# Optimization experiments

Measured on AMD Instinct MI355X. Metric: run time of the kernel, lower is better.

The kernel has to match this reference:

```python
import jax, jax.numpy as jnp
import numpy as np

EPS = 1.0 / 137.0  # fine-structure-constant epsilon used throughout the Yat ops


def yat_dense(x, W, b, alpha):
    # x: [..., C], W: [C, F] -> [..., F]
    dot = jnp.einsum('btc,cf->btf', x, W)
    x_norm = jnp.sum(x * x, axis=-1, keepdims=True)        # [..., 1]
    w_norm = jnp.sum(W * W, axis=0)                         # [F]
    dist = x_norm + w_norm - 2.0 * dot
    y = dot * dot / (dist + EPS)
    y = y + b
    F = W.shape[1]
    scale = (np.sqrt(F) / np.log(1.0 + F)) ** 1.0           # base; alpha exponent applied below
    return y * ((np.float32(np.sqrt(F)) / np.float32(np.log1p(F))) ** alpha)


def setup_inputs() -> dict:
    key = jax.random.key(0)
    ks = jax.random.split(key, 8)
    B, T, C = 4, 1024, 768
    x = jax.random.normal(ks[0], (B, T, C), dtype=jnp.float32)
    mask = jnp.tril(jnp.ones((T, T), dtype=bool))[None, None, :, :]  # causal [1,1,T,T]
    sd = 1.0 / np.sqrt(C)
    W_attn = jax.random.normal(ks[1], (C, 3 * C), dtype=jnp.float32) * sd
    b_attn = jnp.zeros((3 * C,), dtype=jnp.float32)
    alpha_attn = jnp.ones((), dtype=jnp.float32)
    W_proj = jax.random.normal(ks[2], (C, C), dtype=jnp.float32) * sd
    b_proj = jnp.zeros((C,), dtype=jnp.float32)
    alpha_proj = jnp.ones((), dtype=jnp.float32)
    return {"x": x, "mask": mask, "W_attn": W_attn, "b_attn": b_attn,
            "alpha_attn": alpha_attn, "W_proj": W_proj, "b_proj": b_proj,
            "alpha_proj": alpha_proj}


def reference(x, mask, W_attn, b_attn, alpha_attn, W_proj, b_proj, alpha_proj):
    B, T, C = x.shape
    H = 12
    D = C // H  # head_dim
    qkv = yat_dense(x, W_attn, b_attn, alpha_attn)          # [B,T,3C]
    qkv = qkv.reshape(B, T, 3 * H, D)
    q, k, v = jnp.array_split(qkv, 3, axis=2)
    q = jnp.transpose(q, (0, 2, 1, 3))                       # [B,H,T,D]
    k = jnp.transpose(k, (0, 2, 1, 3))
    v = jnp.transpose(v, (0, 2, 1, 3))
    scale = 1.0 / np.float32(np.sqrt(D))
    dot = jnp.einsum('bhid,bhjd->bhij', q, k)                # [B,H,T,T]
    sq_dot = jnp.square(dot * scale)
    q_norm = jnp.sum(jnp.square(q), axis=-1)[..., None]      # [B,H,T,1]
    k_norm = jnp.sum(jnp.square(k), axis=-1)[..., None, :]   # [B,H,1,T]
    sq_dist = q_norm + k_norm - 2.0 * dot * scale
    attn = sq_dot / (sq_dist + EPS)
    attn = jnp.where(mask, attn, jnp.finfo(jnp.float32).min)
    attn = jax.nn.softmax(attn, axis=-1)
    out = jnp.einsum('bhij,bhjd->bhid', attn, v)             # [B,H,T,D]
    out = jnp.transpose(out, (0, 2, 1, 3)).reshape(B, T, C)
    out = yat_dense(out, W_proj, b_proj, alpha_proj)         # [B,T,C]
    return out
```

## Files before the change

kernel.cpp:

```cpp
#include <hip/hip_runtime.h>
#include <math.h>

#define EPS_YAT (1.0f/137.0f)

typedef unsigned short u16;
typedef unsigned int u32;
typedef __attribute__((ext_vector_type(8))) __bf16 bf16x8;
typedef __attribute__((ext_vector_type(4))) float f32x4;

__device__ __forceinline__ float4 ld4(const float* p) { return *(const float4*)p; }

__device__ __forceinline__ u16 bf16_rne(float f) {
    u32 u = __float_as_uint(f);
    u32 r = (u + 0x7fffu + ((u >> 16) & 1u)) >> 16;
    return (u16)r;
}
__device__ __forceinline__ float bf16_f(u16 h) {
    return __uint_as_float(((u32)h) << 16);
}

__device__ __forceinline__ void glds16(const u16* g, u16* s) {
    __builtin_amdgcn_global_load_lds(
        (const __attribute__((address_space(1))) void*)g,
        (__attribute__((address_space(3))) void*)s,
        16, 0, 0);
}

__global__ void colnorm_part(const float* __restrict__ W, float* __restrict__ part,
                             int K, int N) {
    __shared__ float sm[256];
    const int col = blockIdx.x * 64 + (threadIdx.x & 63);
    const int q = threadIdx.x >> 6;
    const int rows = K >> 6;
    const int k0 = blockIdx.y * (K >> 4) + q * rows;
    float s = 0.f;
    for (int k = k0; k < k0 + rows; ++k) {
        float w = W[(size_t)k * N + col];
        s += w * w;
    }
    sm[threadIdx.x] = s;
    __syncthreads();
    if (threadIdx.x < 64)
        part[(size_t)blockIdx.y * N + col] =
            sm[threadIdx.x] + sm[threadIdx.x + 64] + sm[threadIdx.x + 128] + sm[threadIdx.x + 192];
}

__global__ void colnorm_reduce(const float* __restrict__ part, float* __restrict__ wn,
                               int N) {
    int gid = blockIdx.x * 256 + threadIdx.x;
    if (gid >= N) return;
    float s = 0.f;
    #pragma unroll
    for (int i = 0; i < 16; ++i) s += part[(size_t)i * N + gid];
    wn[gid] = s;
}

__global__ void split_rownorm(const float* __restrict__ X, u16* __restrict__ Xh,
                              u16* __restrict__ Xl, float* __restrict__ rn) {
    int wave = threadIdx.x >> 6;
    int lane = threadIdx.x & 63;
    int row = blockIdx.x * 4 + wave;
    const float* xr = X + (size_t)row * 768;
    u16* xh = Xh + (size_t)row * 768;
    u16* xl = Xl + (size_t)row * 768;
    float s = 0.f;
    #pragma unroll
    for (int k = lane * 4; k < 768; k += 256) {
        float4 v = ld4(xr + k);
        s += v.x * v.x + v.y * v.y + v.z * v.z + v.w * v.w;
        u16 h0 = bf16_rne(v.x), h1 = bf16_rne(v.y), h2 = bf16_rne(v.z), h3 = bf16_rne(v.w);
        u16 l0 = bf16_rne(v.x - bf16_f(h0));
        u16 l1 = bf16_rne(v.y - bf16_f(h1));
        u16 l2 = bf16_rne(v.z - bf16_f(h2));
        u16 l3 = bf16_rne(v.w - bf16_f(h3));
        uint2 hp, lp;
        hp.x = (u32)h0 | ((u32)h1 << 16); hp.y = (u32)h2 | ((u32)h3 << 16);
        lp.x = (u32)l0 | ((u32)l1 << 16); lp.y = (u32)l2 | ((u32)l3 << 16);
        *(uint2*)(xh + k) = hp;
        *(uint2*)(xl + k) = lp;
    }
    for (int off = 32; off; off >>= 1) s += __shfl_down(s, off);
    if (lane == 0) rn[row] = s;
}

__global__ void rownorm_hl(const u16* __restrict__ Xh, const u16* __restrict__ Xl,
                           float* __restrict__ rn) {
    int wave = threadIdx.x >> 6;
    int lane = threadIdx.x & 63;
    int row = blockIdx.x * 4 + wave;
    const u16* xh = Xh + (size_t)row * 768;
    const u16* xl = Xl + (size_t)row * 768;
    float s = 0.f;
    for (int k = lane * 4; k < 768; k += 256) {
        uint2 hv = *(const uint2*)(xh + k);
        uint2 lv = *(const uint2*)(xl + k);
        float a0 = bf16_f((u16)hv.x)         + bf16_f((u16)lv.x);
        float a1 = bf16_f((u16)(hv.x >> 16)) + bf16_f((u16)(lv.x >> 16));
        float a2 = bf16_f((u16)hv.y)         + bf16_f((u16)lv.y);
        float a3 = bf16_f((u16)(hv.y >> 16)) + bf16_f((u16)(lv.y >> 16));
        s += a0 * a0 + a1 * a1 + a2 * a2 + a3 * a3;
    }
    for (int off = 32; off; off >>= 1) s += __shfl_down(s, off);
    if (lane == 0) rn[row] = s;
}

__global__ void qknorm_kernel(const u16* __restrict__ qh, const u16* __restrict__ ql,
                              float* __restrict__ qn, float* __restrict__ kn) {
    int gid = blockIdx.x * 256 + threadIdx.x;
    int lane = gid & 15;
    int idx = gid >> 4;
    int which = (idx >= 49152) ? 1 : 0;
    int r = idx - which * 49152;
    int t = r & 1023;
    int bh = r >> 10;
    int h = bh % 12, b = bh / 12;
    const size_t off = (size_t)(b * 1024 + t) * 2304 + which * 768 + h * 64 + lane * 4;
    uint2 hv = *(const uint2*)(qh + off);
    uint2 lv = *(const uint2*)(ql + off);
    float a0 = bf16_f((u16)hv.x)         + bf16_f((u16)lv.x);
    float a1 = bf16_f((u16)(hv.x >> 16)) + bf16_f((u16)(lv.x >> 16));
    float a2 = bf16_f((u16)hv.y)         + bf16_f((u16)lv.y);
    float a3 = bf16_f((u16)(hv.y >> 16)) + bf16_f((u16)(lv.y >> 16));
    float s = a0 * a0 + a1 * a1 + a2 * a2 + a3 * a3;
    s += __shfl_xor(s, 1, 16);
    s += __shfl_xor(s, 2, 16);
    s += __shfl_xor(s, 4, 16);
    s += __shfl_xor(s, 8, 16);
    if (lane == 0) (which ? kn : qn)[r] = s;
}

__global__ void split_wt_kernel(const float* __restrict__ W, u16* __restrict__ Th,
                                u16* __restrict__ Tl, int K, int N) {
    __shared__ float tile[64 * 68];
    const int tid = threadIdx.x;
    const int n0 = blockIdx.x << 6;
    const int k0 = blockIdx.y << 6;
    const int rr = tid >> 4;
    const int cc = (tid & 15) << 2;
    #pragma unroll
    for (int s = 0; s < 4; ++s) {
        int k_l = rr + s * 16;
        *(float4*)&tile[k_l * 68 + cc] = ld4(W + (size_t)(k0 + k_l) * N + n0 + cc);
    }
    __syncthreads();
    #pragma unroll
    for (int s = 0; s < 4; ++s) {
        int n_l = rr + s * 16;
        float a0 = tile[(cc + 0) * 68 + n_l];
        float a1 = tile[(cc + 1) * 68 + n_l];
        float a2 = tile[(cc + 2) * 68 + n_l];
        float a3 = tile[(cc + 3) * 68 + n_l];
        u16 h0 = bf16_rne(a0), h1 = bf16_rne(a1), h2 = bf16_rne(a2), h3 = bf16_rne(a3);
        u16 l0 = bf16_rne(a0 - bf16_f(h0));
        u16 l1 = bf16_rne(a1 - bf16_f(h1));
        u16 l2 = bf16_rne(a2 - bf16_f(h2));
        u16 l3 = bf16_rne(a3 - bf16_f(h3));
        uint2 hp, lp;
        hp.x = (u32)h0 | ((u32)h1 << 16); hp.y = (u32)h2 | ((u32)h3 << 16);
        lp.x = (u32)l0 | ((u32)l1 << 16); lp.y = (u32)l2 | ((u32)l3 << 16);
        size_t o = (size_t)(n0 + n_l) * K + k0 + cc;
        *(uint2*)(Th + o) = hp;
        *(uint2*)(Tl + o) = lp;
    }
}

template<int SPLIT, int NB>
__global__ __launch_bounds__(256, 4)
void yat_gemm_mfma(const u16* __restrict__ Ah, const u16* __restrict__ Al,
                   const u16* __restrict__ Bh, const u16* __restrict__ Bl,
                   const float* __restrict__ bias, const float* __restrict__ xn,
                   const float* __restrict__ wnc, const float* __restrict__ alphap,
                   const float Fdim, float* __restrict__ out,
                   u16* __restrict__ outh, u16* __restrict__ outl,
                   const int N, const int K) {
    __shared__ __align__(16) u16 lds[4096 + NB * 4096];
    const int tid = threadIdx.x;
    const int nwg = gridDim.x * gridDim.y;
    const int orig = blockIdx.y * gridDim.x + blockIdx.x;
    const int swz = (orig & 7) * (nwg >> 3) + (orig >> 3);
    const int m0 = (swz / gridDim.x) << 6;
    const int n0 = (swz % gridDim.x) * (64 * NB);
    const int w = tid >> 6;
    const int l = tid & 63;
    const int lm = l & 15;
    const int kq = l >> 4;
    const int kq4 = kq << 2;
    const int wn = w * 16 * NB;

    const int srow = (w << 4) + (l >> 2);
    const int scol = (l & 3) << 3;
    const u16* gA  = Ah + (size_t)(m0 + srow) * K + scol;
    const u16* gC  = Al + (size_t)(m0 + srow) * K + scol;
    const u16* gB  = Bh + (size_t)(n0 + srow) * K + scol;
    const u16* gD  = Bl + (size_t)(n0 + srow) * K + scol;
    const u16* gB2 = Bh + (size_t)(n0 + 64 + srow) * K + scol;
    const u16* gD2 = Bl + (size_t)(n0 + 64 + srow) * K + scol;
    const int wb = w << 9;

    u16* sAh = lds;
    u16* sAl = lds + 2048;
    u16* sBh = lds + 4096;
    u16* sBl = lds + 4096 + 2048 * NB;

    f32x4 acc[4][NB] = {};

    for (int k0 = 0; k0 < K; k0 += 32) {
        __syncthreads();
        glds16(gA + k0, sAh + wb);
        glds16(gC + k0, sAl + wb);
        glds16(gB + k0, sBh + wb);
        glds16(gD + k0, sBl + wb);
        if constexpr (NB == 2) {
            glds16(gB2 + k0, sBh + 2048 + wb);
            glds16(gD2 + k0, sBl + 2048 + wb);
        }
        __syncthreads();

        bf16x8 fah[4], fal[4], fbh[NB], fbl[NB];
        #pragma unroll
        for (int i = 0; i < 4; ++i) {
            const int ra = (i * 16 + lm) * 32 + (kq << 3);
            fah[i] = *(const bf16x8*)&sAh[ra];
            fal[i] = *(const bf16x8*)&sAl[ra];
        }
        #pragma unroll
        for (int j = 0; j < NB; ++j) {
            const int rb = (wn + j * 16 + lm) * 32 + (kq << 3);
            fbh[j] = *(const bf16x8*)&sBh[rb];
            fbl[j] = *(const bf16x8*)&sBl[rb];
        }
        #pragma unroll
        for (int i = 0; i < 4; ++i)
            #pragma unroll
            for (int j = 0; j < NB; ++j) {
                f32x4 c = acc[i][j];
                c = __builtin_amdgcn_mfma_f32_16x16x32_bf16(fah[i], fbh[j], c, 0, 0, 0);
                c = __builtin_amdgcn_mfma_f32_16x16x32_bf16(fah[i], fbl[j], c, 0, 0, 0);
                c = __builtin_amdgcn_mfma_f32_16x16x32_bf16(fal[i], fbh[j], c, 0, 0, 0);
                acc[i][j] = c;
            }
    }

    const float scale = powf(sqrtf(Fdim) / log1pf(Fdim), *alphap);
    #pragma unroll
    for (int i = 0; i < 4; ++i) {
        const int mbase = m0 + i * 16 + kq4;
        #pragma unroll
        for (int j = 0; j < NB; ++j) {
            const int n = n0 + wn + j * 16 + lm;
            const float w2 = wnc[n];
            const float bv = bias[n];
            #pragma unroll
            for (int r = 0; r < 4; ++r) {
                const int m = mbase + r;
                float d = acc[i][j][r];
                float den = xn[m] + w2 - 2.f * d + EPS_YAT;
                float v = (d * d / den + bv) * scale;
                if constexpr (SPLIT) {
                    u16 hh = bf16_rne(v);
                    outh[(size_t)m * N + n] = hh;
                    outl[(size_t)m * N + n] = bf16_rne(v - bf16_f(hh));
                } else {
                    out[(size_t)m * N + n] = v;
                }
            }
        }
    }
}

#define MFMA_B16(a, b, c) __builtin_amdgcn_mfma_f32_16x16x32_bf16(a, b, c, 0, 0, 0)

#define ST_TILE(j) { \
    const int kro = ((j)*16 + lm) * 72 + (kq << 3); \
    bf16x8 kh = *(const bf16x8*)&KPh[kro]; \
    bf16x8 kl = *(const bf16x8*)&KPl[kro]; \
    st##j = MFMA_B16(kh, qh0, st##j); \
    st##j = MFMA_B16(kl, qh0, st##j); \
    st##j = MFMA_B16(kh, ql0, st##j); \
    kh = *(const bf16x8*)&KPh[kro + 32]; \
    kl = *(const bf16x8*)&KPl[kro + 32]; \
    st##j = MFMA_B16(kh, qh1, st##j); \
    st##j = MFMA_B16(kl, qh1, st##j); \
    st##j = MFMA_B16(kh, ql1, st##j); \
}

#define YAT_EL(j, r) { \
    float sv = st##j[r] * 0.125f; \
    float den = qnm + kns[(j)*16 + kq4 + (r)] - 2.f * sv + EPS_YAT; \
    float v = sv * sv / den; \
    if (diag && ((j)*16 + kq4 + (r) > wband + lm)) v = -3e38f; \
    st##j[r] = v; mm = fmaxf(mm, v); }
#define YAT_TILE(j) YAT_EL(j,0) YAT_EL(j,1) YAT_EL(j,2) YAT_EL(j,3)

#define PEXP_TILE(j) { \
    float p0 = __expf(st##j[0] - mnew), p1 = __expf(st##j[1] - mnew); \
    float p2 = __expf(st##j[2] - mnew), p3 = __expf(st##j[3] - mnew); \
    rs += p0 + p1 + p2 + p3; \
    u16 h0 = bf16_rne(p0), h1 = bf16_rne(p1), h2 = bf16_rne(p2), h3 = bf16_rne(p3); \
    uint2 hp; hp.x = (u32)h0 | ((u32)h1 << 16); hp.y = (u32)h2 | ((u32)h3 << 16); \
    *(uint2*)&KPh[pmrow + (j)*16 + kq4] = hp; \
    u16 e0 = bf16_rne(p0 - bf16_f(h0)), e1 = bf16_rne(p1 - bf16_f(h1)); \
    u16 e2 = bf16_rne(p2 - bf16_f(h2)), e3 = bf16_rne(p3 - bf16_f(h3)); \
    uint2 lp; lp.x = (u32)e0 | ((u32)e1 << 16); lp.y = (u32)e2 | ((u32)e3 << 16); \
    *(uint2*)&KPl[pmrow + (j)*16 + kq4] = lp; }

#define PV_TILE(j) { \
    const int vro = ((j)*16 + lm) * 72 + vkq8; \
    bf16x8 vh = *(const bf16x8*)&Vth[vro]; \
    bf16x8 vl = *(const bf16x8*)&Vtl[vro]; \
    ac##j = MFMA_B16(ph0, vh, ac##j); \
    ac##j = MFMA_B16(pl0, vh, ac##j); \
    ac##j = MFMA_B16(ph0, vl, ac##j); \
    vh = *(const bf16x8*)&Vth[vro + 32]; \
    vl = *(const bf16x8*)&Vtl[vro + 32]; \
    ac##j = MFMA_B16(ph1, vh, ac##j); \
    ac##j = MFMA_B16(pl1, vh, ac##j); \
    ac##j = MFMA_B16(ph1, vl, ac##j); \
}

#define WRVT(dst, v2, m) { \
    dst[(sj * 4 + 16 * (m) + 0) * 72 + toks] = (u16)((v2).x); \
    dst[(sj * 4 + 16 * (m) + 1) * 72 + toks] = (u16)((v2).x >> 16); \
    dst[(sj * 4 + 16 * (m) + 2) * 72 + toks] = (u16)((v2).y); \
    dst[(sj * 4 + 16 * (m) + 3) * 72 + toks] = (u16)((v2).y >> 16); }

__global__ __launch_bounds__(256, 2)
void yat_flash_mfma(const u16* __restrict__ qh_g, const u16* __restrict__ ql_g,
                    const float* __restrict__ qn, const float* __restrict__ kn,
                    u16* __restrict__ outh, u16* __restrict__ outl) {
    __shared__ __align__(16) u16 KPh[64 * 72], KPl[64 * 72];
    __shared__ __align__(16) u16 Vth[64 * 72], Vtl[64 * 72];
    __shared__ float kns[64];

    const int tid = threadIdx.x;
    const int L = blockIdx.x;
    const int u = L / 48;
    const int qt = (u & 1) ? (u >> 1) : (15 - (u >> 1));
    const int bh = L % 48;
    const int h = bh % 12, b = bh / 12;
    const int wave = tid >> 6;
    const int lane = tid & 63;
    const int lm = lane & 15;
    const int kq = lane >> 4;
    const int kq4 = kq << 2;
    const int wband = wave << 4;
    const int sr = tid >> 2;
    const int sj = tid & 3;
    const int toks = sr ^ (sj << 3);
    const int vkq8 = (kq ^ (lm >> 2)) << 3;
    const size_t base = (size_t)(b * 1024) * 2304 + h * 64;

    {
        const size_t qoff = base + (size_t)((qt << 6) + sr) * 2304 + sj * 16;
        *(uint4*)&KPh[sr * 72 + sj * 16]     = *(const uint4*)(qh_g + qoff);
        *(uint4*)&KPh[sr * 72 + sj * 16 + 8] = *(const uint4*)(qh_g + qoff + 8);
        *(uint4*)&KPl[sr * 72 + sj * 16]     = *(const uint4*)(ql_g + qoff);
        *(uint4*)&KPl[sr * 72 + sj * 16 + 8] = *(const uint4*)(ql_g + qoff + 8);
    }
    const float qnm = qn[bh * 1024 + (qt << 6) + wband + lm];

    const size_t r0 = base + (size_t)sr * 2304;
    uint4 kh0 = *(const uint4*)(qh_g + r0 + 768 + sj * 16);
    uint4 kh1 = *(const uint4*)(qh_g + r0 + 768 + sj * 16 + 8);
    uint4 kl0 = *(const uint4*)(ql_g + r0 + 768 + sj * 16);
    uint4 kl1 = *(const uint4*)(ql_g + r0 + 768 + sj * 16 + 8);
    uint2 vh0 = *(const uint2*)(qh_g + r0 + 1536 + sj * 4);
    uint2 vh1 = *(const uint2*)(qh_g + r0 + 1536 + sj * 4 + 16);
    uint2 vh2 = *(const uint2*)(qh_g + r0 + 1536 + sj * 4 + 32);
    uint2 vh3 = *(const uint2*)(qh_g + r0 + 1536 + sj * 4 + 48);
    uint2 vl0 = *(const uint2*)(ql_g + r0 + 1536 + sj * 4);
    uint2 vl1 = *(const uint2*)(ql_g + r0 + 1536 + sj * 4 + 16);
    uint2 vl2 = *(const uint2*)(ql_g + r0 + 1536 + sj * 4 + 32);
    uint2 vl3 = *(const uint2*)(ql_g + r0 + 1536 + sj * 4 + 48);
    float knS = (tid < 64) ? kn[bh * 1024 + tid] : 0.f;

    __syncthreads();

    const int qrow = (wband + lm) * 72;
    const bf16x8 qh0 = *(const bf16x8*)&KPh[qrow + (kq << 3)];
    const bf16x8 qh1 = *(const bf16x8*)&KPh[qrow + 32 + (kq << 3)];
    const bf16x8 ql0 = *(const bf16x8*)&KPl[qrow + (kq << 3)];
    const bf16x8 ql1 = *(const bf16x8*)&KPl[qrow + 32 + (kq << 3)];

    f32x4 ac0 = {}, ac1 = {}, ac2 = {}, ac3 = {};
    float mrun = -3e38f, lrun = 0.f;
    const int pmrow = (wband + lm) * 72;

    for (int kt = 0; kt <= qt; ++kt) {
        __syncthreads();
        *(uint4*)&KPh[sr * 72 + sj * 16]     = kh0;
        *(uint4*)&KPh[sr * 72 + sj * 16 + 8] = kh1;
        *(uint4*)&KPl[sr * 72 + sj * 16]     = kl0;
        *(uint4*)&KPl[sr * 72 + sj * 16 + 8] = kl1;
        WRVT(Vth, vh0, 0) WRVT(Vth, vh1, 1) WRVT(Vth, vh2, 2) WRVT(Vth, vh3, 3)
        WRVT(Vtl, vl0, 0) WRVT(Vtl, vl1, 1) WRVT(Vtl, vl2, 2) WRVT(Vtl, vl3, 3)
        if (tid < 64) kns[tid] = knS;
        __syncthreads();

        if (kt < qt) {
            const size_t r = base + (size_t)(((kt + 1) << 6) + sr) * 2304;
            kh0 = *(const uint4*)(qh_g + r + 768 + sj * 16);
            kh1 = *(const uint4*)(qh_g + r + 768 + sj * 16 + 8);
            kl0 = *(const uint4*)(ql_g + r + 768 + sj * 16);
            kl1 = *(const uint4*)(ql_g + r + 768 + sj * 16 + 8);
            vh0 = *(const uint2*)(qh_g + r + 1536 + sj * 4);
            vh1 = *(const uint2*)(qh_g + r + 1536 + sj * 4 + 16);
            vh2 = *(const uint2*)(qh_g + r + 1536 + sj * 4 + 32);
            vh3 = *(const uint2*)(qh_g + r + 1536 + sj * 4 + 48);
            vl0 = *(const uint2*)(ql_g + r + 1536 + sj * 4);
            vl1 = *(const uint2*)(ql_g + r + 1536 + sj * 4 + 16);
            vl2 = *(const uint2*)(ql_g + r + 1536 + sj * 4 + 32);
            vl3 = *(const uint2*)(ql_g + r + 1536 + sj * 4 + 48);
            if (tid < 64) knS = kn[bh * 1024 + ((kt + 1) << 6) + tid];
        }

        f32x4 st0 = {}, st1 = {}, st2 = {}, st3 = {};
        __builtin_amdgcn_s_setprio(1);
        ST_TILE(0) ST_TILE(1) ST_TILE(2) ST_TILE(3)
        __builtin_amdgcn_s_setprio(0);
        __syncthreads();

        const bool diag = (kt == qt);
        float mm = -3e38f;
        YAT_TILE(0) YAT_TILE(1) YAT_TILE(2) YAT_TILE(3)
        mm = fmaxf(mm, __shfl_xor(mm, 16));
        mm = fmaxf(mm, __shfl_xor(mm, 32));
        const float mnew = fmaxf(mrun, mm);
        const float al = __expf(mrun - mnew);
        mrun = mnew;
        float rs = 0.f;
        PEXP_TILE(0) PEXP_TILE(1) PEXP_TILE(2) PEXP_TILE(3)
        rs += __shfl_xor(rs, 16);
        rs += __shfl_xor(rs, 32);
        lrun = lrun * al + rs;
        const float a0 = __shfl(al, kq4 + 0, 16);
        const float a1 = __shfl(al, kq4 + 1, 16);
        const float a2 = __shfl(al, kq4 + 2, 16);
        const float a3 = __shfl(al, kq4 + 3, 16);
        ac0[0] *= a0; ac0[1] *= a1; ac0[2] *= a2; ac0[3] *= a3;
        ac1[0] *= a0; ac1[1] *= a1; ac1[2] *= a2; ac1[3] *= a3;
        ac2[0] *= a0; ac2[1] *= a1; ac2[2] *= a2; ac2[3] *= a3;
        ac3[0] *= a0; ac3[1] *= a1; ac3[2] *= a2; ac3[3] *= a3;
        __syncthreads();

        const bf16x8 ph0 = *(const bf16x8*)&KPh[pmrow + (kq << 3)];
        const bf16x8 ph1 = *(const bf16x8*)&KPh[pmrow + 32 + (kq << 3)];
        const bf16x8 pl0 = *(const bf16x8*)&KPl[pmrow + (kq << 3)];
        const bf16x8 pl1 = *(const bf16x8*)&KPl[pmrow + 32 + (kq << 3)];
        __builtin_amdgcn_s_setprio(1);
        PV_TILE(0) PV_TILE(1) PV_TILE(2) PV_TILE(3)
        __builtin_amdgcn_s_setprio(0);
    }

    const float i0 = 1.f / __shfl(lrun, kq4 + 0, 16);
    const float i1 = 1.f / __shfl(lrun, kq4 + 1, 16);
    const float i2 = 1.f / __shfl(lrun, kq4 + 2, 16);
    const float i3 = 1.f / __shfl(lrun, kq4 + 3, 16);
    const size_t obase = (size_t)(b * 1024 + (qt << 6) + wband + kq4) * 768 + h * 64 + lm;
    u16* oph = outh + obase;
    u16* opl = outl + obase;
    #define STORE_E(j, r, iv) { \
        float ov = ac##j[r] * iv; \
        u16 hh = bf16_rne(ov); \
        oph[(size_t)(r) * 768 + (j)*16] = hh; \
        opl[(size_t)(r) * 768 + (j)*16] = bf16_rne(ov - bf16_f(hh)); }
    #define STORE_T(j) { STORE_E(j,0,i0) STORE_E(j,1,i1) STORE_E(j,2,i2) STORE_E(j,3,i3) }
    STORE_T(0) STORE_T(1) STORE_T(2) STORE_T(3)
    #undef STORE_T
    #undef STORE_E
}

extern "C" void kernel_launch(void* const* d_in, const int* in_sizes, int n_in,
                              void* d_out, int out_size, void* d_ws, size_t ws_size,
                              hipStream_t stream) {
    const float* x          = (const float*)d_in[0];
    const float* W_attn     = (const float*)d_in[2];
    const float* b_attn     = (const float*)d_in[3];
    const float* alpha_attn = (const float*)d_in[4];
    const float* W_proj     = (const float*)d_in[5];
    const float* b_proj     = (const float*)d_in[6];
    const float* alpha_proj = (const float*)d_in[7];

    float* ws       = (float*)d_ws;
    u16*   qkvh     = (u16*)ws;
    u16*   qkvl     = (u16*)(ws + 4718592);
    float* xn       = ws + 12582912;
    float* an       = ws + 12587008;
    float* wn_attn  = ws + 12591104;
    float* wn_proj  = ws + 12593408;
    float* qn       = ws + 12594176;
    float* kn       = ws + 12643328;

    float* cn_part_a = ws + 9437184;
    float* cn_part_p = ws + 9437184 + 36864;
    u16* xh  = (u16*)(ws + 9437184);
    u16* xl  = (u16*)(ws + 11010048);
    u16* aoh = (u16*)(ws + 9437184);
    u16* aol = (u16*)(ws + 11010048);
    u16* wth = (u16*)d_out;
    u16* wtl = (u16*)d_out + 1769472;
    u16* wph = (u16*)(ws + 3145728);
    u16* wpl = (u16*)(ws + 3440640);

    colnorm_part<<<dim3(36, 16), 256, 0, stream>>>(W_attn, cn_part_a, 768, 2304);
    colnorm_part<<<dim3(12, 16), 256, 0, stream>>>(W_proj, cn_part_p, 768, 768);
    colnorm_reduce<<<9, 256, 0, stream>>>(cn_part_a, wn_attn, 2304);
    colnorm_reduce<<<3, 256, 0, stream>>>(cn_part_p, wn_proj, 768);
    split_rownorm<<<1024, 256, 0, stream>>>(x, xh, xl, xn);
    split_wt_kernel<<<dim3(36, 12), 256, 0, stream>>>(W_attn, wth, wtl, 768, 2304);
    yat_gemm_mfma<1, 2><<<dim3(18, 64), 256, 0, stream>>>(
        xh, xl, wth, wtl, b_attn, xn, wn_attn, alpha_attn, 2304.f,
        nullptr, qkvh, qkvl, 2304, 768);
    qknorm_kernel<<<6144, 256, 0, stream>>>(qkvh, qkvl, qn, kn);
    yat_flash_mfma<<<768, 256, 0, stream>>>(qkvh, qkvl, qn, kn, aoh, aol);
    rownorm_hl<<<1024, 256, 0, stream>>>(aoh, aol, an);
    split_wt_kernel<<<dim3(12, 12), 256, 0, stream>>>(W_proj, wph, wpl, 768, 768);
    yat_gemm_mfma<0, 1><<<dim3(12, 64), 256, 0, stream>>>(
        aoh, aol, wph, wpl, b_proj, an, wn_proj, alpha_proj, 768.f,
        (float*)d_out, nullptr, nullptr, 768, 768);
}
```

Before: 259.2 us.

## Fuse q/k and attention-output row norms into producing kernels, merge colnorm launches

Computes the q/k squared norms in the QKV GEMM epilogue and the attention-output row norms in the flash kernel epilogue, using atomics into a buffer zeroed in the merged colnorm reduce. This removes the separate qknorm and rownorm kernels and their re-reads of the hi/lo bf16 buffers. The two colnorm part and reduce launches are each merged into one. The flash kernel also skips the accumulator rescale when the running max does not change. Norms are now taken from fp32 values before the bf16 split rather than from reconstructed hi+lo values, which shifts rounding slightly, and the atomic sums make the output norms order-dependent.

```diff
diff --git a/kernel.cpp b/kernel.cpp
--- a/kernel.cpp
+++ b/kernel.cpp
@@ -26,15 +26,17 @@
         16, 0, 0);
 }
 
-__global__ void colnorm_part(const float* __restrict__ W, float* __restrict__ part,
-                             int K, int N) {
+__global__ void colnorm_part2(const float* __restrict__ Wa, const float* __restrict__ Wp,
+                              float* __restrict__ pa, float* __restrict__ pp) {
     __shared__ float sm[256];
-    const int col = blockIdx.x * 64 + (threadIdx.x & 63);
+    const float* W; float* part; int N, colbase;
+    if (blockIdx.x < 36) { W = Wa; part = pa; N = 2304; colbase = blockIdx.x * 64; }
+    else                 { W = Wp; part = pp; N = 768;  colbase = (blockIdx.x - 36) * 64; }
+    const int col = colbase + (threadIdx.x & 63);
     const int q = threadIdx.x >> 6;
-    const int rows = K >> 6;
-    const int k0 = blockIdx.y * (K >> 4) + q * rows;
+    const int k0 = blockIdx.y * 48 + q * 12;
     float s = 0.f;
-    for (int k = k0; k < k0 + rows; ++k) {
+    for (int k = k0; k < k0 + 12; ++k) {
         float w = W[(size_t)k * N + col];
         s += w * w;
     }
@@ -45,14 +47,24 @@
             sm[threadIdx.x] + sm[threadIdx.x + 64] + sm[threadIdx.x + 128] + sm[threadIdx.x + 192];
 }
 
-__global__ void colnorm_reduce(const float* __restrict__ part, float* __restrict__ wn,
-                               int N) {
+__global__ void colnorm_reduce2(const float* __restrict__ pa, const float* __restrict__ pp,
+                                float* __restrict__ wa, float* __restrict__ wp,
+                                float* __restrict__ an_zero) {
     int gid = blockIdx.x * 256 + threadIdx.x;
-    if (gid >= N) return;
-    float s = 0.f;
-    #pragma unroll
-    for (int i = 0; i < 16; ++i) s += part[(size_t)i * N + gid];
-    wn[gid] = s;
+    if (gid < 2304) {
+        float s = 0.f;
+        #pragma unroll
+        for (int i = 0; i < 16; ++i) s += pa[(size_t)i * 2304 + gid];
+        wa[gid] = s;
+    } else if (gid < 3072) {
+        int g = gid - 2304;
+        float s = 0.f;
+        #pragma unroll
+        for (int i = 0; i < 16; ++i) s += pp[(size_t)i * 768 + g];
+        wp[g] = s;
+    }
+    int z = gid - 3072;
+    if (z >= 0 && z < 4096) an_zero[z] = 0.f;
 }
 
 __global__ void split_rownorm(const float* __restrict__ X, u16* __restrict__ Xh,
@@ -83,52 +95,6 @@
     if (lane == 0) rn[row] = s;
 }
 
-__global__ void rownorm_hl(const u16* __restrict__ Xh, const u16* __restrict__ Xl,
-                           float* __restrict__ rn) {
-    int wave = threadIdx.x >> 6;
-    int lane = threadIdx.x & 63;
-    int row = blockIdx.x * 4 + wave;
-    const u16* xh = Xh + (size_t)row * 768;
-    const u16* xl = Xl + (size_t)row * 768;
-    float s = 0.f;
-    for (int k = lane * 4; k < 768; k += 256) {
-        uint2 hv = *(const uint2*)(xh + k);
-        uint2 lv = *(const uint2*)(xl + k);
-        float a0 = bf16_f((u16)hv.x)         + bf16_f((u16)lv.x);
-        float a1 = bf16_f((u16)(hv.x >> 16)) + bf16_f((u16)(lv.x >> 16));
-        float a2 = bf16_f((u16)hv.y)         + bf16_f((u16)lv.y);
-        float a3 = bf16_f((u16)(hv.y >> 16)) + bf16_f((u16)(lv.y >> 16));
-        s += a0 * a0 + a1 * a1 + a2 * a2 + a3 * a3;
-    }
-    for (int off = 32; off; off >>= 1) s += __shfl_down(s, off);
-    if (lane == 0) rn[row] = s;
-}
-
-__global__ void qknorm_kernel(const u16* __restrict__ qh, const u16* __restrict__ ql,
-                              float* __restrict__ qn, float* __restrict__ kn) {
-    int gid = blockIdx.x * 256 + threadIdx.x;
-    int lane = gid & 15;
-    int idx = gid >> 4;
-    int which = (idx >= 49152) ? 1 : 0;
-    int r = idx - which * 49152;
-    int t = r & 1023;
-    int bh = r >> 10;
-    int h = bh % 12, b = bh / 12;
-    const size_t off = (size_t)(b * 1024 + t) * 2304 + which * 768 + h * 64 + lane * 4;
-    uint2 hv = *(const uint2*)(qh + off);
-    uint2 lv = *(const uint2*)(ql + off);
-    float a0 = bf16_f((u16)hv.x)         + bf16_f((u16)lv.x);
-    float a1 = bf16_f((u16)(hv.x >> 16)) + bf16_f((u16)(lv.x >> 16));
-    float a2 = bf16_f((u16)hv.y)         + bf16_f((u16)lv.y);
-    float a3 = bf16_f((u16)(hv.y >> 16)) + bf16_f((u16)(lv.y >> 16));
-    float s = a0 * a0 + a1 * a1 + a2 * a2 + a3 * a3;
-    s += __shfl_xor(s, 1, 16);
-    s += __shfl_xor(s, 2, 16);
-    s += __shfl_xor(s, 4, 16);
-    s += __shfl_xor(s, 8, 16);
-    if (lane == 0) (which ? kn : qn)[r] = s;
-}
-
 __global__ void split_wt_kernel(const float* __restrict__ W, u16* __restrict__ Th,
                                 u16* __restrict__ Tl, int K, int N) {
     __shared__ float tile[64 * 68];
@@ -172,6 +138,7 @@
                    const float* __restrict__ wnc, const float* __restrict__ alphap,
                    const float Fdim, float* __restrict__ out,
                    u16* __restrict__ outh, u16* __restrict__ outl,
+                   float* __restrict__ qn, float* __restrict__ kn,
                    const int N, const int K) {
     __shared__ __align__(16) u16 lds[4096 + NB * 4096];
     const int tid = threadIdx.x;
@@ -242,9 +209,12 @@
     }
 
     const float scale = powf(sqrtf(Fdim) / log1pf(Fdim), *alphap);
+    float pp[4][4];
     #pragma unroll
     for (int i = 0; i < 4; ++i) {
         const int mbase = m0 + i * 16 + kq4;
+        #pragma unroll
+        for (int r = 0; r < 4; ++r) pp[i][r] = 0.f;
         #pragma unroll
         for (int j = 0; j < NB; ++j) {
             const int n = n0 + wn + j * 16 + lm;
@@ -260,9 +230,41 @@
                     u16 hh = bf16_rne(v);
                     outh[(size_t)m * N + n] = hh;
                     outl[(size_t)m * N + n] = bf16_rne(v - bf16_f(hh));
+                    pp[i][r] += v * v;
                 } else {
                     out[(size_t)m * N + n] = v;
                 }
+            }
+        }
+    }
+
+    if constexpr (SPLIT) {
+        if (n0 < 1536) {
+            __syncthreads();
+            float* red = (float*)lds;
+            #pragma unroll
+            for (int i = 0; i < 4; ++i)
+                #pragma unroll
+                for (int r = 0; r < 4; ++r) {
+                    float s = pp[i][r];
+                    s += __shfl_xor(s, 1, 16);
+                    s += __shfl_xor(s, 2, 16);
+                    s += __shfl_xor(s, 4, 16);
+                    s += __shfl_xor(s, 8, 16);
+                    if (lm == 0) red[w * 64 + i * 16 + kq4 + r] = s;
+                }
+            __syncthreads();
+            if (tid < 128) {
+                const int hh = tid >> 6;
+                const int ml = tid & 63;
+                const float s = red[(2 * hh) * 64 + ml] + red[(2 * hh + 1) * 64 + ml];
+                const int m = m0 + ml;
+                const int b = m >> 10, t = m & 1023;
+                const int hcol = n0 + hh * 64;
+                if (hcol < 768)
+                    qn[(b * 12 + (hcol >> 6)) * 1024 + t] = s;
+                else
+                    kn[(b * 12 + ((hcol - 768) >> 6)) * 1024 + t] = s;
             }
         }
     }
@@ -327,7 +329,8 @@
 __global__ __launch_bounds__(256, 2)
 void yat_flash_mfma(const u16* __restrict__ qh_g, const u16* __restrict__ ql_g,
                     const float* __restrict__ qn, const float* __restrict__ kn,
-                    u16* __restrict__ outh, u16* __restrict__ outl) {
+                    u16* __restrict__ outh, u16* __restrict__ outl,
+                    float* __restrict__ an_g) {
     __shared__ __align__(16) u16 KPh[64 * 72], KPl[64 * 72];
     __shared__ __align__(16) u16 Vth[64 * 72], Vtl[64 * 72];
     __shared__ float kns[64];
@@ -426,21 +429,24 @@
         mm = fmaxf(mm, __shfl_xor(mm, 16));
         mm = fmaxf(mm, __shfl_xor(mm, 32));
         const float mnew = fmaxf(mrun, mm);
-        const float al = __expf(mrun - mnew);
+        if (!__all(mm <= mrun)) {
+            const float al = __expf(mrun - mnew);
+            const float a0 = __shfl(al, kq4 + 0, 16);
+            const float a1 = __shfl(al, kq4 + 1, 16);
+            const float a2 = __shfl(al, kq4 + 2, 16);
+            const float a3 = __shfl(al, kq4 + 3, 16);
+            ac0[0] *= a0; ac0[1] *= a1; ac0[2] *= a2; ac0[3] *= a3;
+            ac1[0] *= a0; ac1[1] *= a1; ac1[2] *= a2; ac1[3] *= a3;
+            ac2[0] *= a0; ac2[1] *= a1; ac2[2] *= a2; ac2[3] *= a3;
+            ac3[0] *= a0; ac3[1] *= a1; ac3[2] *= a2; ac3[3] *= a3;
+            lrun *= al;
+        }
         mrun = mnew;
         float rs = 0.f;
         PEXP_TILE(0) PEXP_TILE(1) PEXP_TILE(2) PEXP_TILE(3)
         rs += __shfl_xor(rs, 16);
         rs += __shfl_xor(rs, 32);
-        lrun = lrun * al + rs;
-        const float a0 = __shfl(al, kq4 + 0, 16);
-        const float a1 = __shfl(al, kq4 + 1, 16);
-        const float a2 = __shfl(al, kq4 + 2, 16);
-        const float a3 = __shfl(al, kq4 + 3, 16);
-        ac0[0] *= a0; ac0[1] *= a1; ac0[2] *= a2; ac0[3] *= a3;
-        ac1[0] *= a0; ac1[1] *= a1; ac1[2] *= a2; ac1[3] *= a3;
-        ac2[0] *= a0; ac2[1] *= a1; ac2[2] *= a2; ac2[3] *= a3;
-        ac3[0] *= a0; ac3[1] *= a1; ac3[2] *= a2; ac3[3] *= a3;
+        lrun += rs;
         __syncthreads();
 
         const bf16x8 ph0 = *(const bf16x8*)&KPh[pmrow + (kq << 3)];
@@ -459,8 +465,10 @@
     const size_t obase = (size_t)(b * 1024 + (qt << 6) + wband + kq4) * 768 + h * 64 + lm;
     u16* oph = outh + obase;
     u16* opl = outl + obase;
+    float rsum0 = 0.f, rsum1 = 0.f, rsum2 = 0.f, rsum3 = 0.f;
     #define STORE_E(j, r, iv) { \
         float ov = ac##j[r] * iv; \
+        rsum##r += ov * ov; \
         u16 hh = bf16_rne(ov); \
         oph[(size_t)(r) * 768 + (j)*16] = hh; \
         opl[(size_t)(r) * 768 + (j)*16] = bf16_rne(ov - bf16_f(hh)); }
@@ -468,6 +476,16 @@
     STORE_T(0) STORE_T(1) STORE_T(2) STORE_T(3)
     #undef STORE_T
     #undef STORE_E
+    const int arow = b * 1024 + (qt << 6) + wband + kq4;
+    #define REDROW(r) { \
+        float s = rsum##r; \
+        s += __shfl_xor(s, 1, 16); \
+        s += __shfl_xor(s, 2, 16); \
+        s += __shfl_xor(s, 4, 16); \
+        s += __shfl_xor(s, 8, 16); \
+        if (lm == 0) atomicAdd(&an_g[arow + (r)], s); }
+    REDROW(0) REDROW(1) REDROW(2) REDROW(3)
+    #undef REDROW
 }
 
 extern "C" void kernel_launch(void* const* d_in, const int* in_sizes, int n_in,
@@ -502,20 +520,16 @@
     u16* wph = (u16*)(ws + 3145728);
     u16* wpl = (u16*)(ws + 3440640);
 
-    colnorm_part<<<dim3(36, 16), 256, 0, stream>>>(W_attn, cn_part_a, 768, 2304);
-    colnorm_part<<<dim3(12, 16), 256, 0, stream>>>(W_proj, cn_part_p, 768, 768);
-    colnorm_reduce<<<9, 256, 0, stream>>>(cn_part_a, wn_attn, 2304);
-    colnorm_reduce<<<3, 256, 0, stream>>>(cn_part_p, wn_proj, 768);
+    colnorm_part2<<<dim3(48, 16), 256, 0, stream>>>(W_attn, W_proj, cn_part_a, cn_part_p);
+    colnorm_reduce2<<<28, 256, 0, stream>>>(cn_part_a, cn_part_p, wn_attn, wn_proj, an);
     split_rownorm<<<1024, 256, 0, stream>>>(x, xh, xl, xn);
     split_wt_kernel<<<dim3(36, 12), 256, 0, stream>>>(W_attn, wth, wtl, 768, 2304);
     yat_gemm_mfma<1, 2><<<dim3(18, 64), 256, 0, stream>>>(
         xh, xl, wth, wtl, b_attn, xn, wn_attn, alpha_attn, 2304.f,
-        nullptr, qkvh, qkvl, 2304, 768);
-    qknorm_kernel<<<6144, 256, 0, stream>>>(qkvh, qkvl, qn, kn);
-    yat_flash_mfma<<<768, 256, 0, stream>>>(qkvh, qkvl, qn, kn, aoh, aol);
-    rownorm_hl<<<1024, 256, 0, stream>>>(aoh, aol, an);
+        nullptr, qkvh, qkvl, qn, kn, 2304, 768);
+    yat_flash_mfma<<<768, 256, 0, stream>>>(qkvh, qkvl, qn, kn, aoh, aol, an);
     split_wt_kernel<<<dim3(12, 12), 256, 0, stream>>>(W_proj, wph, wpl, 768, 768);
     yat_gemm_mfma<0, 1><<<dim3(12, 64), 256, 0, stream>>>(
         aoh, aol, wph, wpl, b_proj, an, wn_proj, alpha_proj, 768.f,
-        (float*)d_out, nullptr, nullptr, 768, 768);
-}
+        (float*)d_out, nullptr, nullptr, nullptr, nullptr, 768, 768);
+}
```

Result: faster. 248.0 us (-4.3%).
